# Kernel optimization log

Hardware: AMD Instinct MI355X
Metric: run time of the kernel (lower is better)

The kernel has to match this reference:

```python
import jax, jax.numpy as jnp
import numpy as np

N_NODES = 100000
N_EDGES = 500000
D_IN = 128
D_HID = 256
D_OUT = 1


def mish(x):
    # x * tanh(softplus(x))
    return x * jnp.tanh(jax.nn.softplus(x))


def setup_inputs() -> dict:
    key = jax.random.key(0)
    k1, k2, k3, k4, k5, k6 = jax.random.split(key, 6)
    z = jax.random.normal(k1, (N_NODES, D_IN), dtype=jnp.float32)
    edge = jax.random.randint(k2, (2, N_EDGES), 0, N_NODES, dtype=jnp.int64)
    # PyTorch Linear default init: U(-1/sqrt(fan_in), 1/sqrt(fan_in))
    s1 = 1.0 / np.sqrt(D_IN)
    s2 = 1.0 / np.sqrt(D_HID)
    W1 = jax.random.uniform(k3, (D_HID, D_IN), minval=-s1, maxval=s1, dtype=jnp.float32)
    b1 = jax.random.uniform(k4, (D_HID,), minval=-s1, maxval=s1, dtype=jnp.float32)
    W2 = jax.random.uniform(k5, (D_OUT, D_HID), minval=-s2, maxval=s2, dtype=jnp.float32)
    b2 = jax.random.uniform(k6, (D_OUT,), minval=-s2, maxval=s2, dtype=jnp.float32)
    return {"z": z, "edge": edge, "W1": W1, "b1": b1, "W2": W2, "b2": b2}


def reference(z, edge, W1, b1, W2, b2):
    # gather node pairs and elementwise product: [E, D_IN]
    x = z[edge[0]] * z[edge[1]]
    # fc1 + mish (dropout is identity in eval mode)
    h = mish(jnp.einsum('ed,hd->eh', x, W1) + b1)
    # fc2 + sigmoid -> [E, 1]
    logits = jnp.einsum('eh,oh->eo', h, W2) + b2
    return jax.nn.sigmoid(logits)
```

## Files before the change

kernel.cpp:

```cpp
#include <hip/hip_runtime.h>
#include <hip/hip_bf16.h>
#include <hip/hip_fp16.h>
#include <type_traits>


#define N_NODES 100000
#define N_EDGES 500000
#define D_IN    128
#define D_HID   256
#define M_TILE  32
#define NTILES  (N_EDGES / M_TILE)
#define LDS_STRIDE 136
#define GRID    1024

typedef _Float16 half8  __attribute__((ext_vector_type(8)));
typedef __bf16   bf16x8 __attribute__((ext_vector_type(8)));
typedef float    f32x4  __attribute__((ext_vector_type(4)));
typedef float    f32x2  __attribute__((ext_vector_type(2)));

union F4H { float4 v; f32x2 h[2]; };

__device__ __forceinline__ unsigned int pkbf(f32x2 q) {
    union { __hip_bfloat162 b; unsigned int u; } c;
    c.b = __float22bfloat162_rn(make_float2(q.x, q.y));
    return c.u;
}

__device__ __forceinline__ f32x2 mish2(f32x2 x) {
    f32x2 xc = {fminf(x.x, 20.0f), fminf(x.y, 20.0f)};
    f32x2 E  = {__expf(xc.x), __expf(xc.y)};
    f32x2 num = E * (E + 2.0f);
    f32x2 den = num + 2.0f;
    f32x2 r  = {__builtin_amdgcn_rcpf(den.x), __builtin_amdgcn_rcpf(den.y)};
    return x * num * r;
}

__global__ __launch_bounds__(256)
void zcvt_kernel(const float* __restrict__ z, _Float16* __restrict__ zh) {
    const size_t i = (size_t)blockIdx.x * 256 + threadIdx.x;
    const float4 f0 = *reinterpret_cast<const float4*>(z + i * 8);
    const float4 f1 = *reinterpret_cast<const float4*>(z + i * 8 + 4);
    union { half8 h; uint4 u; } o;
    o.h[0] = (_Float16)f0.x; o.h[1] = (_Float16)f0.y;
    o.h[2] = (_Float16)f0.z; o.h[3] = (_Float16)f0.w;
    o.h[4] = (_Float16)f1.x; o.h[5] = (_Float16)f1.y;
    o.h[6] = (_Float16)f1.z; o.h[7] = (_Float16)f1.w;
    *reinterpret_cast<uint4*>(zh + i * 8) = o.u;
}

template <bool USE_H>
__global__ __launch_bounds__(512, 4)
void edge_decoder_kernel(const float*    __restrict__ z,
                         const _Float16* __restrict__ zh,
                         const int*      __restrict__ edge,
                         const float*    __restrict__ W1,
                         const float*    __restrict__ b1,
                         const float*    __restrict__ W2,
                         const float*    __restrict__ b2,
                         float*          __restrict__ out) {
    using frag_t = std::conditional_t<USE_H, half8, bf16x8>;

    __shared__ ushort xbuf[2][M_TILE * LDS_STRIDE];
    __shared__ float  lpart[2][8][M_TILE];

    const int t    = threadIdx.x;
    const int wave = t >> 6;
    const int lane = t & 63;
    const int quad = lane >> 4;
    const int nlo  = lane & 15;

    frag_t bfrag[4][2];
    #pragma unroll
    for (int nt = 0; nt < 2; ++nt) {
        const int n = wave * 32 + nt * 16 + nlo;
        const float* wrow = W1 + n * D_IN;
        #pragma unroll
        for (int ks = 0; ks < 4; ++ks) {
            float4 w0 = *reinterpret_cast<const float4*>(wrow + ks * 32 + quad * 8);
            float4 w1 = *reinterpret_cast<const float4*>(wrow + ks * 32 + quad * 8 + 4);
            float wa[8] = {w0.x, w0.y, w0.z, w0.w, w1.x, w1.y, w1.z, w1.w};
            if constexpr (USE_H) {
                half8 hv;
                #pragma unroll
                for (int j = 0; j < 8; ++j) hv[j] = (_Float16)wa[j];
                bfrag[ks][nt] = hv;
            } else {
                bf16x8 bv;
                #pragma unroll
                for (int j = 0; j < 8; ++j) bv[j] = (__bf16)wa[j];
                bfrag[ks][nt] = bv;
            }
        }
    }
    f32x2 b1p[2][2], w2p[2][2];
    #pragma unroll
    for (int nt = 0; nt < 2; ++nt) {
        const int nb = wave * 32 + nt * 16 + quad * 4;
        b1p[nt][0] = (f32x2){b1[nb],     b1[nb + 1]};
        b1p[nt][1] = (f32x2){b1[nb + 2], b1[nb + 3]};
        w2p[nt][0] = (f32x2){W2[nb],     W2[nb + 1]};
        w2p[nt][1] = (f32x2){W2[nb + 2], W2[nb + 3]};
    }
    const float b2f = b2[0];

    const int s_slot = t >> 4;
    const int cch    = t & 15;

    int tile = blockIdx.x;
    float4 a0, a1, c0, c1;
    half8  ha, hc;
    {
        const int e = tile * M_TILE + s_slot;
        const int u = edge[e], v = edge[N_EDGES + e];
        if constexpr (USE_H) {
            ha = *reinterpret_cast<const half8*>(zh + (size_t)u * D_IN + cch * 8);
            hc = *reinterpret_cast<const half8*>(zh + (size_t)v * D_IN + cch * 8);
        } else {
            const float* zu = z + (size_t)u * D_IN + cch * 8;
            const float* zv = z + (size_t)v * D_IN + cch * 8;
            a0 = *reinterpret_cast<const float4*>(zu);
            a1 = *reinterpret_cast<const float4*>(zu + 4);
            c0 = *reinterpret_cast<const float4*>(zv);
            c1 = *reinterpret_cast<const float4*>(zv + 4);
        }
    }
    int u_n, v_n;
    {
        const int t1 = min(tile + GRID, NTILES - 1);
        const int e1 = t1 * M_TILE + s_slot;
        if constexpr (USE_H) {
            u_n = edge[e1] * 256 + cch * 16;
            v_n = edge[N_EDGES + e1] * 256 + cch * 16;
        } else {
            u_n = edge[e1]; v_n = edge[N_EDGES + e1];
        }
    }

    int  p = 0;
    bool have_prev = false;
    int  prev_base = 0;

    for (; tile < NTILES; tile += GRID) {
        if constexpr (USE_H) {
            union { half8 h; uint4 u; } pr;
            pr.h = ha * hc;
            *reinterpret_cast<uint4*>(&xbuf[p][s_slot * LDS_STRIDE + cch * 8]) = pr.u;
        } else {
            F4H A0{a0}, A1{a1}, C0{c0}, C1{c1};
            unsigned int r0 = pkbf(A0.h[0] * C0.h[0]);
            unsigned int r1 = pkbf(A0.h[1] * C0.h[1]);
            unsigned int r2 = pkbf(A1.h[0] * C1.h[0]);
            unsigned int r3 = pkbf(A1.h[1] * C1.h[1]);
            *reinterpret_cast<uint4*>(&xbuf[p][s_slot * LDS_STRIDE + cch * 8]) =
                make_uint4(r0, r1, r2, r3);
        }
        __syncthreads();

        if constexpr (USE_H) {
            ha = *reinterpret_cast<const half8*>(
                     reinterpret_cast<const char*>(zh) + u_n);
            hc = *reinterpret_cast<const half8*>(
                     reinterpret_cast<const char*>(zh) + v_n);
        } else {
            const float* zu = z + (size_t)u_n * D_IN + cch * 8;
            const float* zv = z + (size_t)v_n * D_IN + cch * 8;
            a0 = *reinterpret_cast<const float4*>(zu);
            a1 = *reinterpret_cast<const float4*>(zu + 4);
            c0 = *reinterpret_cast<const float4*>(zv);
            c1 = *reinterpret_cast<const float4*>(zv + 4);
        }
        {
            const int t2 = min(tile + 2 * GRID, NTILES - 1);
            const int e2 = t2 * M_TILE + s_slot;
            if constexpr (USE_H) {
                u_n = edge[e2] * 256 + cch * 16;
                v_n = edge[N_EDGES + e2] * 256 + cch * 16;
            } else {
                u_n = edge[e2]; v_n = edge[N_EDGES + e2];
            }
        }

        if (have_prev) {
            if (t < M_TILE) {
                const int pp = p ^ 1;
                float logit = b2f;
                #pragma unroll
                for (int w = 0; w < 8; ++w) logit += lpart[pp][w][t];
                out[prev_base + t] = __builtin_amdgcn_rcpf(1.0f + __expf(-logit));
            }
        }

        f32x4 acc[2][2];
        #pragma unroll
        for (int mt = 0; mt < 2; ++mt)
            #pragma unroll
            for (int nt = 0; nt < 2; ++nt)
                acc[mt][nt] = (f32x4){0.f, 0.f, 0.f, 0.f};

        #pragma unroll
        for (int ks = 0; ks < 4; ++ks) {
            frag_t af[2];
            #pragma unroll
            for (int mt = 0; mt < 2; ++mt)
                af[mt] = *reinterpret_cast<const frag_t*>(
                    &xbuf[p][(mt * 16 + nlo) * LDS_STRIDE + ks * 32 + quad * 8]);
            #pragma unroll
            for (int mt = 0; mt < 2; ++mt)
                #pragma unroll
                for (int nt = 0; nt < 2; ++nt) {
                    if constexpr (USE_H)
                        acc[mt][nt] = __builtin_amdgcn_mfma_f32_16x16x32_f16(
                            bfrag[ks][nt], af[mt], acc[mt][nt], 0, 0, 0);
                    else
                        acc[mt][nt] = __builtin_amdgcn_mfma_f32_16x16x32_bf16(
                            bfrag[ks][nt], af[mt], acc[mt][nt], 0, 0, 0);
                }
        }

        #pragma unroll
        for (int mt = 0; mt < 2; ++mt) {
            f32x2 dot = {0.f, 0.f};
            #pragma unroll
            for (int nt = 0; nt < 2; ++nt) {
                f32x2 h0 = (f32x2){acc[mt][nt][0], acc[mt][nt][1]} + b1p[nt][0];
                f32x2 h1 = (f32x2){acc[mt][nt][2], acc[mt][nt][3]} + b1p[nt][1];
                f32x2 m0 = mish2(h0);
                f32x2 m1 = mish2(h1);
                dot += m0 * w2p[nt][0];
                dot += m1 * w2p[nt][1];
            }
            float s = dot.x + dot.y;
            s += __shfl_xor(s, 16);
            s += __shfl_xor(s, 32);
            if (quad == 0) lpart[p][wave][mt * 16 + nlo] = s;
        }

        have_prev = true;
        prev_base = tile * M_TILE;
        p ^= 1;
    }

    __syncthreads();
    if (have_prev && t < M_TILE) {
        const int pp = p ^ 1;
        float logit = b2f;
        #pragma unroll
        for (int w = 0; w < 8; ++w) logit += lpart[pp][w][t];
        out[prev_base + t] = __builtin_amdgcn_rcpf(1.0f + __expf(-logit));
    }
}

extern "C" void kernel_launch(void* const* d_in, const int* in_sizes, int n_in,
                              void* d_out, int out_size, void* d_ws, size_t ws_size,
                              hipStream_t stream) {
    const float* z    = (const float*)d_in[0];
    const int*   edge = (const int*)d_in[1];
    const float* W1   = (const float*)d_in[2];
    const float* b1   = (const float*)d_in[3];
    const float* W2   = (const float*)d_in[4];
    const float* b2   = (const float*)d_in[5];
    float* out = (float*)d_out;

    const size_t zh_bytes = (size_t)N_NODES * D_IN * sizeof(_Float16);
    if (d_ws != nullptr && ws_size >= zh_bytes) {
        _Float16* zh = (_Float16*)d_ws;
        zcvt_kernel<<<dim3(N_NODES * D_IN / 8 / 256), dim3(256), 0, stream>>>(z, zh);
        edge_decoder_kernel<true><<<dim3(GRID), dim3(512), 0, stream>>>(
            z, zh, edge, W1, b1, W2, b2, out);
    } else {
        edge_decoder_kernel<false><<<dim3(GRID), dim3(512), 0, stream>>>(
            z, nullptr, edge, W1, b1, W2, b2, out);
    }
}
```

Baseline: 165.9 us.

## Compute Mish epilogue in packed fp16 and move barrier after prefetch

The bias add, Mish activation and fc2 dot-product epilogue now run in packed half precision, using the hardware f16 exp and rcp instructions with a lower clamp, instead of fp32. This is meant to halve the transcendental and VALU cost of the per-edge activation. The block barrier also moves after the next tile's gather loads are issued, so those global loads overlap the barrier wait. The trade-off is reduced accuracy: fp16 accumulation of the dot products and a clamp at 5 rather than 20 may shift outputs near tolerance.

```diff
diff --git a/kernel.cpp b/kernel.cpp
--- a/kernel.cpp
+++ b/kernel.cpp
@@ -14,6 +14,8 @@
 #define GRID    1024
 
 typedef _Float16 half8  __attribute__((ext_vector_type(8)));
+typedef _Float16 h2     __attribute__((ext_vector_type(2)));
+typedef __fp16   fp16x2 __attribute__((ext_vector_type(2)));
 typedef __bf16   bf16x8 __attribute__((ext_vector_type(8)));
 typedef float    f32x4  __attribute__((ext_vector_type(4)));
 typedef float    f32x2  __attribute__((ext_vector_type(2)));
@@ -26,12 +28,30 @@
     return c.u;
 }
 
-__device__ __forceinline__ f32x2 mish2(f32x2 x) {
-    f32x2 xc = {fminf(x.x, 20.0f), fminf(x.y, 20.0f)};
-    f32x2 E  = {__expf(xc.x), __expf(xc.y)};
-    f32x2 num = E * (E + 2.0f);
-    f32x2 den = num + 2.0f;
-    f32x2 r  = {__builtin_amdgcn_rcpf(den.x), __builtin_amdgcn_rcpf(den.y)};
+__device__ __forceinline__ h2 pkh(float a, float b) {
+    fp16x2 r = __builtin_amdgcn_cvt_pkrtz(a, b);
+    return __builtin_bit_cast(h2, r);
+}
+
+__device__ __forceinline__ _Float16 exp2h(_Float16 x) {
+    _Float16 r; asm("v_exp_f16 %0, %1" : "=v"(r) : "v"(x)); return r;
+}
+__device__ __forceinline__ _Float16 rcph(_Float16 x) {
+    _Float16 r; asm("v_rcp_f16 %0, %1" : "=v"(r) : "v"(x)); return r;
+}
+
+__device__ __forceinline__ h2 mish_h2(h2 x) {
+    const _Float16 k5 = (_Float16)5.0f;
+    h2 xc;
+    xc.x = x.x < k5 ? x.x : k5;
+    xc.y = x.y < k5 ? x.y : k5;
+    h2 xs = xc * (_Float16)1.44269504f;
+    h2 E;
+    E.x = exp2h(xs.x); E.y = exp2h(xs.y);
+    h2 num = E * (E + (_Float16)2.0f);
+    h2 den = num + (_Float16)2.0f;
+    h2 r;
+    r.x = rcph(den.x); r.y = rcph(den.y);
     return x * num * r;
 }
 
@@ -92,14 +112,14 @@
             }
         }
     }
-    f32x2 b1p[2][2], w2p[2][2];
+    h2 b1h[2][2], w2h[2][2];
     #pragma unroll
     for (int nt = 0; nt < 2; ++nt) {
         const int nb = wave * 32 + nt * 16 + quad * 4;
-        b1p[nt][0] = (f32x2){b1[nb],     b1[nb + 1]};
-        b1p[nt][1] = (f32x2){b1[nb + 2], b1[nb + 3]};
-        w2p[nt][0] = (f32x2){W2[nb],     W2[nb + 1]};
-        w2p[nt][1] = (f32x2){W2[nb + 2], W2[nb + 3]};
+        b1h[nt][0] = (h2){(_Float16)b1[nb],     (_Float16)b1[nb + 1]};
+        b1h[nt][1] = (h2){(_Float16)b1[nb + 2], (_Float16)b1[nb + 3]};
+        w2h[nt][0] = (h2){(_Float16)W2[nb],     (_Float16)W2[nb + 1]};
+        w2h[nt][1] = (h2){(_Float16)W2[nb + 2], (_Float16)W2[nb + 3]};
     }
     const float b2f = b2[0];
 
@@ -154,7 +174,6 @@
             *reinterpret_cast<uint4*>(&xbuf[p][s_slot * LDS_STRIDE + cch * 8]) =
                 make_uint4(r0, r1, r2, r3);
         }
-        __syncthreads();
 
         if constexpr (USE_H) {
             ha = *reinterpret_cast<const half8*>(
@@ -180,6 +199,8 @@
             }
         }
 
+        __syncthreads();
+
         if (have_prev) {
             if (t < M_TILE) {
                 const int pp = p ^ 1;
@@ -219,17 +240,15 @@
 
         #pragma unroll
         for (int mt = 0; mt < 2; ++mt) {
-            f32x2 dot = {0.f, 0.f};
+            h2 dot = (h2){(_Float16)0.0f, (_Float16)0.0f};
             #pragma unroll
             for (int nt = 0; nt < 2; ++nt) {
-                f32x2 h0 = (f32x2){acc[mt][nt][0], acc[mt][nt][1]} + b1p[nt][0];
-                f32x2 h1 = (f32x2){acc[mt][nt][2], acc[mt][nt][3]} + b1p[nt][1];
-                f32x2 m0 = mish2(h0);
-                f32x2 m1 = mish2(h1);
-                dot += m0 * w2p[nt][0];
-                dot += m1 * w2p[nt][1];
-            }
-            float s = dot.x + dot.y;
+                h2 x0 = pkh(acc[mt][nt][0], acc[mt][nt][1]) + b1h[nt][0];
+                h2 x1 = pkh(acc[mt][nt][2], acc[mt][nt][3]) + b1h[nt][1];
+                dot += mish_h2(x0) * w2h[nt][0];
+                dot += mish_h2(x1) * w2h[nt][1];
+            }
+            float s = (float)dot.x + (float)dot.y;
             s += __shfl_xor(s, 16);
             s += __shfl_xor(s, 32);
             if (quad == 0) lpart[p][wave][mt * 16 + nlo] = s;
```

Result: no change. 165.5 us (-0.2%).

## Use 1024-thread blocks with 16 waves each owning 16 hidden columns

Applied to the files above, without the earlier changes.

Doubles the threads per block to 1024 (16 waves) and halves the grid. Each wave now owns 16 hidden units instead of 32, so each thread does half the MFMA and mish work and gathers 4 features per edge instead of 8. The __syncthreads is moved after the next-tile gathers are issued, so those loads overlap with the barrier. The intent is more memory-level parallelism and latency hiding for the random gathers, at the cost of a larger cross-wave reduction (16 partials) and larger block-level barriers.

```diff
diff --git a/kernel.cpp b/kernel.cpp
--- a/kernel.cpp
+++ b/kernel.cpp
@@ -11,9 +11,11 @@
 #define M_TILE  32
 #define NTILES  (N_EDGES / M_TILE)
 #define LDS_STRIDE 136
-#define GRID    1024
+#define GRID    512
+#define NWAVES  16
 
 typedef _Float16 half8  __attribute__((ext_vector_type(8)));
+typedef _Float16 half4  __attribute__((ext_vector_type(4)));
 typedef __bf16   bf16x8 __attribute__((ext_vector_type(8)));
 typedef float    f32x4  __attribute__((ext_vector_type(4)));
 typedef float    f32x2  __attribute__((ext_vector_type(2)));
@@ -49,7 +51,7 @@
 }
 
 template <bool USE_H>
-__global__ __launch_bounds__(512, 4)
+__global__ __launch_bounds__(1024, 8)
 void edge_decoder_kernel(const float*    __restrict__ z,
                          const _Float16* __restrict__ zh,
                          const int*      __restrict__ edge,
@@ -61,7 +63,7 @@
     using frag_t = std::conditional_t<USE_H, half8, bf16x8>;
 
     __shared__ ushort xbuf[2][M_TILE * LDS_STRIDE];
-    __shared__ float  lpart[2][8][M_TILE];
+    __shared__ float  lpart[2][NWAVES][M_TILE];
 
     const int t    = threadIdx.x;
     const int wave = t >> 6;
@@ -69,10 +71,9 @@
     const int quad = lane >> 4;
     const int nlo  = lane & 15;
 
-    frag_t bfrag[4][2];
-    #pragma unroll
-    for (int nt = 0; nt < 2; ++nt) {
-        const int n = wave * 32 + nt * 16 + nlo;
+    frag_t bfrag[4];
+    {
+        const int n = wave * 16 + nlo;
         const float* wrow = W1 + n * D_IN;
         #pragma unroll
         for (int ks = 0; ks < 4; ++ks) {
@@ -83,45 +84,40 @@
                 half8 hv;
                 #pragma unroll
                 for (int j = 0; j < 8; ++j) hv[j] = (_Float16)wa[j];
-                bfrag[ks][nt] = hv;
+                bfrag[ks] = hv;
             } else {
                 bf16x8 bv;
                 #pragma unroll
                 for (int j = 0; j < 8; ++j) bv[j] = (__bf16)wa[j];
-                bfrag[ks][nt] = bv;
-            }
-        }
-    }
-    f32x2 b1p[2][2], w2p[2][2];
-    #pragma unroll
-    for (int nt = 0; nt < 2; ++nt) {
-        const int nb = wave * 32 + nt * 16 + quad * 4;
-        b1p[nt][0] = (f32x2){b1[nb],     b1[nb + 1]};
-        b1p[nt][1] = (f32x2){b1[nb + 2], b1[nb + 3]};
-        w2p[nt][0] = (f32x2){W2[nb],     W2[nb + 1]};
-        w2p[nt][1] = (f32x2){W2[nb + 2], W2[nb + 3]};
+                bfrag[ks] = bv;
+            }
+        }
+    }
+    f32x2 b1p[2], w2p[2];
+    {
+        const int nb = wave * 16 + quad * 4;
+        b1p[0] = (f32x2){b1[nb],     b1[nb + 1]};
+        b1p[1] = (f32x2){b1[nb + 2], b1[nb + 3]};
+        w2p[0] = (f32x2){W2[nb],     W2[nb + 1]};
+        w2p[1] = (f32x2){W2[nb + 2], W2[nb + 3]};
     }
     const float b2f = b2[0];
 
-    const int s_slot = t >> 4;
-    const int cch    = t & 15;
+    const int s_slot = t >> 5;
+    const int cch    = t & 31;
 
     int tile = blockIdx.x;
-    float4 a0, a1, c0, c1;
-    half8  ha, hc;
+    float4 a0, c0;
+    half4  ha, hc;
     {
         const int e = tile * M_TILE + s_slot;
         const int u = edge[e], v = edge[N_EDGES + e];
         if constexpr (USE_H) {
-            ha = *reinterpret_cast<const half8*>(zh + (size_t)u * D_IN + cch * 8);
-            hc = *reinterpret_cast<const half8*>(zh + (size_t)v * D_IN + cch * 8);
-        } else {
-            const float* zu = z + (size_t)u * D_IN + cch * 8;
-            const float* zv = z + (size_t)v * D_IN + cch * 8;
-            a0 = *reinterpret_cast<const float4*>(zu);
-            a1 = *reinterpret_cast<const float4*>(zu + 4);
-            c0 = *reinterpret_cast<const float4*>(zv);
-            c1 = *reinterpret_cast<const float4*>(zv + 4);
+            ha = *reinterpret_cast<const half4*>(zh + (size_t)u * D_IN + cch * 4);
+            hc = *reinterpret_cast<const half4*>(zh + (size_t)v * D_IN + cch * 4);
+        } else {
+            a0 = *reinterpret_cast<const float4*>(z + (size_t)u * D_IN + cch * 4);
+            c0 = *reinterpret_cast<const float4*>(z + (size_t)v * D_IN + cch * 4);
         }
     }
     int u_n, v_n;
@@ -129,8 +125,8 @@
         const int t1 = min(tile + GRID, NTILES - 1);
         const int e1 = t1 * M_TILE + s_slot;
         if constexpr (USE_H) {
-            u_n = edge[e1] * 256 + cch * 16;
-            v_n = edge[N_EDGES + e1] * 256 + cch * 16;
+            u_n = edge[e1] * 256 + cch * 8;
+            v_n = edge[N_EDGES + e1] * 256 + cch * 8;
         } else {
             u_n = edge[e1]; v_n = edge[N_EDGES + e1];
         }
@@ -142,60 +138,52 @@
 
     for (; tile < NTILES; tile += GRID) {
         if constexpr (USE_H) {
-            union { half8 h; uint4 u; } pr;
+            union { half4 h; uint2 u; } pr;
             pr.h = ha * hc;
-            *reinterpret_cast<uint4*>(&xbuf[p][s_slot * LDS_STRIDE + cch * 8]) = pr.u;
-        } else {
-            F4H A0{a0}, A1{a1}, C0{c0}, C1{c1};
+            *reinterpret_cast<uint2*>(&xbuf[p][s_slot * LDS_STRIDE + cch * 4]) = pr.u;
+        } else {
+            F4H A0{a0}, C0{c0};
             unsigned int r0 = pkbf(A0.h[0] * C0.h[0]);
             unsigned int r1 = pkbf(A0.h[1] * C0.h[1]);
-            unsigned int r2 = pkbf(A1.h[0] * C1.h[0]);
-            unsigned int r3 = pkbf(A1.h[1] * C1.h[1]);
-            *reinterpret_cast<uint4*>(&xbuf[p][s_slot * LDS_STRIDE + cch * 8]) =
-                make_uint4(r0, r1, r2, r3);
-        }
-        __syncthreads();
-
-        if constexpr (USE_H) {
-            ha = *reinterpret_cast<const half8*>(
+            *reinterpret_cast<uint2*>(&xbuf[p][s_slot * LDS_STRIDE + cch * 4]) =
+                make_uint2(r0, r1);
+        }
+
+        if constexpr (USE_H) {
+            ha = *reinterpret_cast<const half4*>(
                      reinterpret_cast<const char*>(zh) + u_n);
-            hc = *reinterpret_cast<const half8*>(
+            hc = *reinterpret_cast<const half4*>(
                      reinterpret_cast<const char*>(zh) + v_n);
         } else {
-            const float* zu = z + (size_t)u_n * D_IN + cch * 8;
-            const float* zv = z + (size_t)v_n * D_IN + cch * 8;
-            a0 = *reinterpret_cast<const float4*>(zu);
-            a1 = *reinterpret_cast<const float4*>(zu + 4);
-            c0 = *reinterpret_cast<const float4*>(zv);
-            c1 = *reinterpret_cast<const float4*>(zv + 4);
+            a0 = *reinterpret_cast<const float4*>(z + (size_t)u_n * D_IN + cch * 4);
+            c0 = *reinterpret_cast<const float4*>(z + (size_t)v_n * D_IN + cch * 4);
         }
         {
             const int t2 = min(tile + 2 * GRID, NTILES - 1);
             const int e2 = t2 * M_TILE + s_slot;
             if constexpr (USE_H) {
-                u_n = edge[e2] * 256 + cch * 16;
-                v_n = edge[N_EDGES + e2] * 256 + cch * 16;
+                u_n = edge[e2] * 256 + cch * 8;
+                v_n = edge[N_EDGES + e2] * 256 + cch * 8;
             } else {
                 u_n = edge[e2]; v_n = edge[N_EDGES + e2];
             }
         }
+
+        __syncthreads();
 
         if (have_prev) {
             if (t < M_TILE) {
                 const int pp = p ^ 1;
                 float logit = b2f;
                 #pragma unroll
-                for (int w = 0; w < 8; ++w) logit += lpart[pp][w][t];
+                for (int w = 0; w < NWAVES; ++w) logit += lpart[pp][w][t];
                 out[prev_base + t] = __builtin_amdgcn_rcpf(1.0f + __expf(-logit));
             }
         }
 
-        f32x4 acc[2][2];
-        #pragma unroll
-        for (int mt = 0; mt < 2; ++mt)
-            #pragma unroll
-            for (int nt = 0; nt < 2; ++nt)
-                acc[mt][nt] = (f32x4){0.f, 0.f, 0.f, 0.f};
+        f32x4 acc[2];
+        acc[0] = (f32x4){0.f, 0.f, 0.f, 0.f};
+        acc[1] = (f32x4){0.f, 0.f, 0.f, 0.f};
 
         #pragma unroll
         for (int ks = 0; ks < 4; ++ks) {
@@ -205,30 +193,23 @@
                 af[mt] = *reinterpret_cast<const frag_t*>(
                     &xbuf[p][(mt * 16 + nlo) * LDS_STRIDE + ks * 32 + quad * 8]);
             #pragma unroll
-            for (int mt = 0; mt < 2; ++mt)
-                #pragma unroll
-                for (int nt = 0; nt < 2; ++nt) {
-                    if constexpr (USE_H)
-                        acc[mt][nt] = __builtin_amdgcn_mfma_f32_16x16x32_f16(
-                            bfrag[ks][nt], af[mt], acc[mt][nt], 0, 0, 0);
-                    else
-                        acc[mt][nt] = __builtin_amdgcn_mfma_f32_16x16x32_bf16(
-                            bfrag[ks][nt], af[mt], acc[mt][nt], 0, 0, 0);
-                }
+            for (int mt = 0; mt < 2; ++mt) {
+                if constexpr (USE_H)
+                    acc[mt] = __builtin_amdgcn_mfma_f32_16x16x32_f16(
+                        bfrag[ks], af[mt], acc[mt], 0, 0, 0);
+                else
+                    acc[mt] = __builtin_amdgcn_mfma_f32_16x16x32_bf16(
+                        bfrag[ks], af[mt], acc[mt], 0, 0, 0);
+            }
         }
 
         #pragma unroll
         for (int mt = 0; mt < 2; ++mt) {
-            f32x2 dot = {0.f, 0.f};
-            #pragma unroll
-            for (int nt = 0; nt < 2; ++nt) {
-                f32x2 h0 = (f32x2){acc[mt][nt][0], acc[mt][nt][1]} + b1p[nt][0];
-                f32x2 h1 = (f32x2){acc[mt][nt][2], acc[mt][nt][3]} + b1p[nt][1];
-                f32x2 m0 = mish2(h0);
-                f32x2 m1 = mish2(h1);
-                dot += m0 * w2p[nt][0];
-                dot += m1 * w2p[nt][1];
-            }
+            f32x2 h0 = (f32x2){acc[mt][0], acc[mt][1]} + b1p[0];
+            f32x2 h1 = (f32x2){acc[mt][2], acc[mt][3]} + b1p[1];
+            f32x2 m0 = mish2(h0);
+            f32x2 m1 = mish2(h1);
+            f32x2 dot = m0 * w2p[0] + m1 * w2p[1];
             float s = dot.x + dot.y;
             s += __shfl_xor(s, 16);
             s += __shfl_xor(s, 32);
@@ -245,7 +226,7 @@
         const int pp = p ^ 1;
         float logit = b2f;
         #pragma unroll
-        for (int w = 0; w < 8; ++w) logit += lpart[pp][w][t];
+        for (int w = 0; w < NWAVES; ++w) logit += lpart[pp][w][t];
         out[prev_base + t] = __builtin_amdgcn_rcpf(1.0f + __expf(-logit));
     }
 }
@@ -265,10 +246,10 @@
     if (d_ws != nullptr && ws_size >= zh_bytes) {
         _Float16* zh = (_Float16*)d_ws;
         zcvt_kernel<<<dim3(N_NODES * D_IN / 8 / 256), dim3(256), 0, stream>>>(z, zh);
-        edge_decoder_kernel<true><<<dim3(GRID), dim3(512), 0, stream>>>(
+        edge_decoder_kernel<true><<<dim3(GRID), dim3(1024), 0, stream>>>(
             z, zh, edge, W1, b1, W2, b2, out);
     } else {
-        edge_decoder_kernel<false><<<dim3(GRID), dim3(512), 0, stream>>>(
+        edge_decoder_kernel<false><<<dim3(GRID), dim3(1024), 0, stream>>>(
             z, nullptr, edge, W1, b1, W2, b2, out);
     }
 }
```

New measurement: 176.6 us. 1.06x slower.
